# Optimization experiments

Measured on AMD Instinct MI355X. Metric: run time of the kernel, lower is better.

The kernel has to match this reference:

```python
import jax, jax.numpy as jnp
import numpy as np

INPUT_CHANNELS = 64
OUT_CHANNELS = 64
OUT_DIM = 4
IN_FEAT = INPUT_CHANNELS * OUT_DIM * 2   # 512
OUT_FEAT = OUT_CHANNELS * OUT_DIM        # 256
BATCH = 65536


def setup_inputs() -> dict:
    key = jax.random.key(0)
    k_x, k_w, k_b = jax.random.split(key, 3)
    x = jax.random.normal(k_x, (BATCH, IN_FEAT), dtype=jnp.float32)
    weight = jax.random.normal(k_w, (OUT_FEAT, IN_FEAT), dtype=jnp.float32)
    bias = jax.random.normal(k_b, (1, OUT_FEAT), dtype=jnp.float32)
    return {"x": x, "weight": weight, "bias": bias}


def reference(x, weight, bias) -> jnp.ndarray:
    # Original: (x[:, None] * weight).sum(-1) / sqrt(input_channels) + 0.1*bias
    # Mathematically identical to a GEMM: x @ weight.T
    scale = 1.0 / jnp.sqrt(jnp.asarray(INPUT_CHANNELS, dtype=x.dtype))
    out = jnp.einsum('bi,oi->bo', x, weight) * scale  # [B, out_feat]
    out = out + bias * 0.1
    return out
```

## Files before the change

### kernel.cpp

```cpp
#include <hip/hip_runtime.h>
#include <hip/hip_bf16.h>


typedef __bf16 bf16;
typedef __attribute__((ext_vector_type(8))) __bf16 bf16x8;
typedef __attribute__((ext_vector_type(4))) __bf16 bf16x4;
typedef __attribute__((ext_vector_type(4))) float f32x4;

#define BATCH_ 65536
#define KDIM   512
#define NDIM   256
#define CHUNK_ROWS 16
#define CHUNKS 16
#define ROWS_PER_BLOCK (CHUNK_ROWS * CHUNKS)
#define CHUNK_BYTES (CHUNK_ROWS * KDIM * 4)

__global__ __launch_bounds__(256) void wcvt_kernel(const float* __restrict__ w,
                                                   bf16* __restrict__ wb) {
    int i = (blockIdx.x * 256 + threadIdx.x) * 4;
    f32x4 v = *(const f32x4*)(w + i);
    bf16x4 o;
    o[0] = (bf16)(v.x * 0.125f);
    o[1] = (bf16)(v.y * 0.125f);
    o[2] = (bf16)(v.z * 0.125f);
    o[3] = (bf16)(v.w * 0.125f);
    *(bf16x4*)(wb + i) = o;
}

__device__ __forceinline__ void stage_chunk(const float* xc, float* buf, int tid) {
#pragma unroll
    for (int p = 0; p < 4; ++p) {
        const char* g = (const char*)xc + p * 8192 + tid * 16;
        char* l = (char*)buf + p * 8192 + (tid >> 6) * 1024;
        __builtin_amdgcn_global_load_lds(
            (const __attribute__((address_space(1))) void*)g,
            (__attribute__((address_space(3))) void*)l, 16, 0, 0);
    }
}

__device__ __forceinline__ bf16x8 cvt_a(f32x4 lo, f32x4 hi) {
    bf16x8 a;
    a[0] = (bf16)lo.x; a[1] = (bf16)lo.y; a[2] = (bf16)lo.z; a[3] = (bf16)lo.w;
    a[4] = (bf16)hi.x; a[5] = (bf16)hi.y; a[6] = (bf16)hi.z; a[7] = (bf16)hi.w;
    return a;
}

__device__ __forceinline__ void compute_chunk(const float* buf,
                                              const bf16x8 (&wf)[16][2],
                                              int l16, int q, f32x4 (&acc)[2]) {
    acc[0] = (f32x4)0.0f;
    acc[1] = (f32x4)0.0f;
    const float* rowp = buf + l16 * KDIM + q * 8;
#pragma unroll
    for (int kc = 0; kc < 16; ++kc) {
        f32x4 lo = *(const f32x4*)(rowp + kc * 32);
        f32x4 hi = *(const f32x4*)(rowp + kc * 32 + 4);
        bf16x8 a = cvt_a(lo, hi);
        acc[0] = __builtin_amdgcn_mfma_f32_16x16x32_bf16(a, wf[kc][0], acc[0], 0, 0, 0);
        acc[1] = __builtin_amdgcn_mfma_f32_16x16x32_bf16(a, wf[kc][1], acc[1], 0, 0, 0);
    }
}

__global__ __launch_bounds__(512, 2) void gemm_kernel(const float* __restrict__ x,
                                                      const bf16* __restrict__ wb,
                                                      const float* __restrict__ bias,
                                                      float* __restrict__ out) {
    __shared__ __align__(16) float bufA[CHUNK_ROWS * KDIM];
    __shared__ __align__(16) float bufB[CHUNK_ROWS * KDIM];

    const int tid  = threadIdx.x;
    const int lane = tid & 63;
    const int w    = tid >> 6;
    const int q    = lane >> 4;
    const int l16  = lane & 15;
    const int n0   = w * 32;
    const long row_base = (long)blockIdx.x * ROWS_PER_BLOCK;

    bf16x8 wf[16][2];
#pragma unroll
    for (int kc = 0; kc < 16; ++kc)
#pragma unroll
        for (int nt = 0; nt < 2; ++nt)
            wf[kc][nt] = *(const bf16x8*)(wb + (long)(n0 + nt * 16 + l16) * KDIM
                                             + kc * 32 + q * 8);
    float bv[2];
    bv[0] = 0.1f * bias[n0 + l16];
    bv[1] = 0.1f * bias[n0 + 16 + l16];

    const float* xblk = x + row_base * KDIM;

    stage_chunk(xblk, bufA, tid);
    __syncthreads();

    f32x4 acc[2];
#pragma unroll 1
    for (int t = 0; t < CHUNKS; t += 2) {
        if (t + 1 < CHUNKS)
            stage_chunk(xblk + (long)(t + 1) * CHUNK_ROWS * KDIM, bufB, tid);
        compute_chunk(bufA, wf, l16, q, acc);
        __syncthreads();
        {
            const long row0 = row_base + (long)t * CHUNK_ROWS;
#pragma unroll
            for (int nt = 0; nt < 2; ++nt)
#pragma unroll
                for (int r = 0; r < 4; ++r)
                    out[(row0 + q * 4 + r) * NDIM + n0 + nt * 16 + l16] = acc[nt][r] + bv[nt];
        }

        if (t + 2 < CHUNKS)
            stage_chunk(xblk + (long)(t + 2) * CHUNK_ROWS * KDIM, bufA, tid);
        compute_chunk(bufB, wf, l16, q, acc);
        __syncthreads();
        {
            const long row0 = row_base + (long)(t + 1) * CHUNK_ROWS;
#pragma unroll
            for (int nt = 0; nt < 2; ++nt)
#pragma unroll
                for (int r = 0; r < 4; ++r)
                    out[(row0 + q * 4 + r) * NDIM + n0 + nt * 16 + l16] = acc[nt][r] + bv[nt];
        }
    }
}

extern "C" void kernel_launch(void* const* d_in, const int* in_sizes, int n_in,
                              void* d_out, int out_size, void* d_ws, size_t ws_size,
                              hipStream_t stream) {
    const float* x    = (const float*)d_in[0];
    const float* w    = (const float*)d_in[1];
    const float* bias = (const float*)d_in[2];
    float* out = (float*)d_out;
    bf16* wb   = (bf16*)d_ws;

    wcvt_kernel<<<(NDIM * KDIM) / (256 * 4), 256, 0, stream>>>(w, wb);
    gemm_kernel<<<BATCH_ / ROWS_PER_BLOCK, 512, 0, stream>>>(x, wb, bias, out);
}
```

Baseline: 230.4 us.

## Split N across blocks, convert x to bf16 once into swizzled LDS

The grid is split so each block handles 128 output columns and half as many rows, giving four times as many blocks. Occupancy goes up (launch bounds 512,4), and each wave needs only one MFMA accumulator and half the weight registers. X tiles now pass through registers and are converted to bf16 once when written to LDS, with an XOR swizzle to avoid bank conflicts. This replaces the old scheme where every wave re-converted fp32 rows read from LDS. The cost is that each x row is fetched from global memory twice, once per column half, and the async global-to-LDS load is replaced by register staging.

```diff
diff --git a/kernel.cpp b/kernel.cpp
--- a/kernel.cpp
+++ b/kernel.cpp
@@ -10,10 +10,10 @@
 #define BATCH_ 65536
 #define KDIM   512
 #define NDIM   256
+#define NHALF  128
 #define CHUNK_ROWS 16
-#define CHUNKS 16
+#define CHUNKS 8
 #define ROWS_PER_BLOCK (CHUNK_ROWS * CHUNKS)
-#define CHUNK_BYTES (CHUNK_ROWS * KDIM * 4)
 
 __global__ __launch_bounds__(256) void wcvt_kernel(const float* __restrict__ w,
                                                    bf16* __restrict__ wb) {
@@ -27,98 +27,99 @@
     *(bf16x4*)(wb + i) = o;
 }
 
-__device__ __forceinline__ void stage_chunk(const float* xc, float* buf, int tid) {
+__device__ __forceinline__ void stage_issue(const float* xc, int tid, f32x4 (&r)[4]) {
 #pragma unroll
-    for (int p = 0; p < 4; ++p) {
-        const char* g = (const char*)xc + p * 8192 + tid * 16;
-        char* l = (char*)buf + p * 8192 + (tid >> 6) * 1024;
-        __builtin_amdgcn_global_load_lds(
-            (const __attribute__((address_space(1))) void*)g,
-            (__attribute__((address_space(3))) void*)l, 16, 0, 0);
+    for (int i = 0; i < 4; ++i)
+        r[i] = *(const f32x4*)((const char*)xc + i * 8192 + tid * 16);
+}
+
+__device__ __forceinline__ void stage_write(bf16* buf, int tid, const f32x4 (&r)[4]) {
+#pragma unroll
+    for (int i = 0; i < 4; ++i) {
+        const int row = i * 4 + (tid >> 7);
+        const int off = (tid & 127) * 8;
+        const int phys = row * 1024 + (off ^ ((row & 7) << 4));
+        bf16x4 o;
+        o[0] = (bf16)r[i].x;
+        o[1] = (bf16)r[i].y;
+        o[2] = (bf16)r[i].z;
+        o[3] = (bf16)r[i].w;
+        *(bf16x4*)((char*)buf + phys) = o;
     }
 }
 
-__device__ __forceinline__ bf16x8 cvt_a(f32x4 lo, f32x4 hi) {
-    bf16x8 a;
-    a[0] = (bf16)lo.x; a[1] = (bf16)lo.y; a[2] = (bf16)lo.z; a[3] = (bf16)lo.w;
-    a[4] = (bf16)hi.x; a[5] = (bf16)hi.y; a[6] = (bf16)hi.z; a[7] = (bf16)hi.w;
-    return a;
-}
-
-__device__ __forceinline__ void compute_chunk(const float* buf,
-                                              const bf16x8 (&wf)[16][2],
-                                              int l16, int q, f32x4 (&acc)[2]) {
-    acc[0] = (f32x4)0.0f;
-    acc[1] = (f32x4)0.0f;
-    const float* rowp = buf + l16 * KDIM + q * 8;
+__device__ __forceinline__ void compute_chunk(const bf16* buf, const bf16x8 (&wf)[16],
+                                              int l16, int q, f32x4& acc) {
+    acc = (f32x4)0.0f;
+    const char* base = (const char*)buf + l16 * 1024;
+    const int xo = (l16 & 7) << 4;
 #pragma unroll
     for (int kc = 0; kc < 16; ++kc) {
-        f32x4 lo = *(const f32x4*)(rowp + kc * 32);
-        f32x4 hi = *(const f32x4*)(rowp + kc * 32 + 4);
-        bf16x8 a = cvt_a(lo, hi);
-        acc[0] = __builtin_amdgcn_mfma_f32_16x16x32_bf16(a, wf[kc][0], acc[0], 0, 0, 0);
-        acc[1] = __builtin_amdgcn_mfma_f32_16x16x32_bf16(a, wf[kc][1], acc[1], 0, 0, 0);
+        bf16x8 a = *(const bf16x8*)(base + ((kc * 64 + q * 16) ^ xo));
+        acc = __builtin_amdgcn_mfma_f32_16x16x32_bf16(a, wf[kc], acc, 0, 0, 0);
     }
 }
 
-__global__ __launch_bounds__(512, 2) void gemm_kernel(const float* __restrict__ x,
+__global__ __launch_bounds__(512, 4) void gemm_kernel(const float* __restrict__ x,
                                                       const bf16* __restrict__ wb,
                                                       const float* __restrict__ bias,
                                                       float* __restrict__ out) {
-    __shared__ __align__(16) float bufA[CHUNK_ROWS * KDIM];
-    __shared__ __align__(16) float bufB[CHUNK_ROWS * KDIM];
+    __shared__ __align__(16) bf16 bufA[CHUNK_ROWS * KDIM];
+    __shared__ __align__(16) bf16 bufB[CHUNK_ROWS * KDIM];
 
     const int tid  = threadIdx.x;
     const int lane = tid & 63;
     const int w    = tid >> 6;
     const int q    = lane >> 4;
     const int l16  = lane & 15;
-    const int n0   = w * 32;
-    const long row_base = (long)blockIdx.x * ROWS_PER_BLOCK;
+    const int half = blockIdx.x & 1;
+    const long rb  = blockIdx.x >> 1;
+    const int n0   = half * NHALF + w * 16;
+    const long row_base = rb * ROWS_PER_BLOCK;
 
-    bf16x8 wf[16][2];
+    bf16x8 wf[16];
 #pragma unroll
     for (int kc = 0; kc < 16; ++kc)
-#pragma unroll
-        for (int nt = 0; nt < 2; ++nt)
-            wf[kc][nt] = *(const bf16x8*)(wb + (long)(n0 + nt * 16 + l16) * KDIM
-                                             + kc * 32 + q * 8);
-    float bv[2];
-    bv[0] = 0.1f * bias[n0 + l16];
-    bv[1] = 0.1f * bias[n0 + 16 + l16];
+        wf[kc] = *(const bf16x8*)(wb + (long)(n0 + l16) * KDIM + kc * 32 + q * 8);
+    const float bv = 0.1f * bias[n0 + l16];
 
     const float* xblk = x + row_base * KDIM;
 
-    stage_chunk(xblk, bufA, tid);
+    {
+        f32x4 r0[4];
+        stage_issue(xblk, tid, r0);
+        stage_write(bufA, tid, r0);
+    }
     __syncthreads();
 
-    f32x4 acc[2];
+    f32x4 acc;
+    f32x4 r[4];
 #pragma unroll 1
     for (int t = 0; t < CHUNKS; t += 2) {
         if (t + 1 < CHUNKS)
-            stage_chunk(xblk + (long)(t + 1) * CHUNK_ROWS * KDIM, bufB, tid);
+            stage_issue(xblk + (long)(t + 1) * CHUNK_ROWS * KDIM, tid, r);
         compute_chunk(bufA, wf, l16, q, acc);
+        if (t + 1 < CHUNKS)
+            stage_write(bufB, tid, r);
         __syncthreads();
         {
             const long row0 = row_base + (long)t * CHUNK_ROWS;
 #pragma unroll
-            for (int nt = 0; nt < 2; ++nt)
-#pragma unroll
-                for (int r = 0; r < 4; ++r)
-                    out[(row0 + q * 4 + r) * NDIM + n0 + nt * 16 + l16] = acc[nt][r] + bv[nt];
+            for (int rr = 0; rr < 4; ++rr)
+                out[(row0 + q * 4 + rr) * NDIM + n0 + l16] = acc[rr] + bv;
         }
 
         if (t + 2 < CHUNKS)
-            stage_chunk(xblk + (long)(t + 2) * CHUNK_ROWS * KDIM, bufA, tid);
+            stage_issue(xblk + (long)(t + 2) * CHUNK_ROWS * KDIM, tid, r);
         compute_chunk(bufB, wf, l16, q, acc);
+        if (t + 2 < CHUNKS)
+            stage_write(bufA, tid, r);
         __syncthreads();
         {
             const long row0 = row_base + (long)(t + 1) * CHUNK_ROWS;
 #pragma unroll
-            for (int nt = 0; nt < 2; ++nt)
-#pragma unroll
-                for (int r = 0; r < 4; ++r)
-                    out[(row0 + q * 4 + r) * NDIM + n0 + nt * 16 + l16] = acc[nt][r] + bv[nt];
+            for (int rr = 0; rr < 4; ++rr)
+                out[(row0 + q * 4 + rr) * NDIM + n0 + l16] = acc[rr] + bv;
         }
     }
 }
@@ -133,5 +134,5 @@
     bf16* wb   = (bf16*)d_ws;
 
     wcvt_kernel<<<(NDIM * KDIM) / (256 * 4), 256, 0, stream>>>(w, wb);
-    gemm_kernel<<<BATCH_ / ROWS_PER_BLOCK, 512, 0, stream>>>(x, wb, bias, out);
+    gemm_kernel<<<(BATCH_ / ROWS_PER_BLOCK) * 2, 512, 0, stream>>>(x, wb, bias, out);
 }
```

Measured after the change: 230.2 us. Within noise of the previous version (-0.1%).
